# Performance work log

Measured on AMD Instinct MI355X. Metric: run time of the kernel, lower is better.

## Reference

```python
import jax, jax.numpy as jnp
import numpy as np

B, S = 2, 2048
HID, NH, NKV, HD = 4096, 32, 8, 128
THETA = 10000.0
WINDOW = 1024  # sliding window size


def setup_inputs() -> dict:
    key = jax.random.key(0)
    k1, k2, k3 = jax.random.split(key, 3)
    hidden_states = jax.random.normal(k1, (B, S, HID), jnp.float32)
    wqkv = jax.random.normal(k2, (HID, (NH + 2 * NKV) * HD), jnp.float32) * 0.02
    wo = jax.random.normal(k3, (NH * HD, HID), jnp.float32) * 0.02
    positions = jnp.arange(S, dtype=jnp.int32)
    return {"hidden_states": hidden_states, "wqkv": wqkv, "wo": wo, "positions": positions}


def _rope_neox(x, positions):
    # x: [B, S, h, HD]; GPT-NeoX style: rotate concatenated halves.
    half = HD // 2
    inv_freq = 1.0 / (THETA ** (jnp.arange(half, dtype=jnp.float32) / half))
    ang = positions.astype(jnp.float32)[:, None] * inv_freq  # [S, half]
    cos = jnp.cos(ang)[None, :, None, :]
    sin = jnp.sin(ang)[None, :, None, :]
    x1, x2 = jnp.split(x, 2, axis=-1)
    return jnp.concatenate([x1 * cos - x2 * sin, x2 * cos + x1 * sin], axis=-1)


def reference(hidden_states, wqkv, wo, positions):
    qkv = hidden_states @ wqkv  # [B, S, (NH+2*NKV)*HD]
    q, k, v = jnp.split(qkv, [NH * HD, NH * HD + NKV * HD], axis=-1)
    q = q.reshape(B, S, NH, HD)
    k = k.reshape(B, S, NKV, HD)
    v = v.reshape(B, S, NKV, HD)
    q = _rope_neox(q, positions)
    k = _rope_neox(k, positions)
    # GQA: each KV head serves NH // NKV query heads
    rep = NH // NKV
    k = jnp.repeat(k, rep, axis=2)  # [B, S, NH, HD]
    v = jnp.repeat(v, rep, axis=2)
    scale = HD ** -0.5
    scores = jnp.einsum('bqhd,bkhd->bhqk', q, k) * scale  # [B, NH, S, S]
    i = jnp.arange(S)[:, None]
    j = jnp.arange(S)[None, :]
    mask = (j <= i) & (i - j < WINDOW)  # causal + sliding window
    scores = jnp.where(mask[None, None], scores, jnp.float32(-1e30))
    probs = jax.nn.softmax(scores, axis=-1)
    attn = jnp.einsum('bhqk,bkhd->bqhd', probs, v).reshape(B, S, NH * HD)
    return attn @ wo  # [B, S, HID]
```

## Files before the change

kernel.cpp:

```cpp
#include <hip/hip_runtime.h>


typedef __attribute__((ext_vector_type(8))) short short8;
typedef __attribute__((ext_vector_type(4))) float f32x4;
typedef __attribute__((ext_vector_type(16))) float f32x16;
typedef __attribute__((ext_vector_type(4))) unsigned int u32x4;
typedef __attribute__((ext_vector_type(4))) unsigned short u16x4;

__device__ __forceinline__ unsigned short f2bf(float f) {
  unsigned int u = __builtin_bit_cast(unsigned int, f);
  u = u + 0x7fffu + ((u >> 16) & 1u);
  return (unsigned short)(u >> 16);
}
__device__ __forceinline__ float bf2f(unsigned short h) {
  unsigned int u = ((unsigned int)h) << 16;
  return __builtin_bit_cast(float, u);
}
__device__ __forceinline__ unsigned int cvtpk_bf16(float lo, float hi) {
  unsigned int r;
  asm("v_cvt_pk_bf16_f32 %0, %1, %2" : "=v"(r) : "v"(lo), "v"(hi));
  return r;
}

__device__ __forceinline__ void gload_lds16(const unsigned short* g, unsigned short* l) {
  __builtin_amdgcn_global_load_lds(
      (const __attribute__((address_space(1))) unsigned int*)g,
      (__attribute__((address_space(3))) unsigned int*)l, 16, 0, 0);
}

#define MFMA16(A, B, C) __builtin_amdgcn_mfma_f32_16x16x32_bf16((A), (B), (C), 0, 0, 0)
#define MFMA32(A, B, C) __builtin_amdgcn_mfma_f32_32x32x16_bf16((A), (B), (C), 0, 0, 0)
#define BC8(x) __builtin_bit_cast(short8, (x))

__global__ __launch_bounds__(256) void cvt_plain(const float* __restrict__ in,
                                                 unsigned short* __restrict__ out, int n) {
  const int i = (blockIdx.x * 256 + threadIdx.x) * 4;
  (void)n;
  f32x4 v = *(const f32x4*)(in + i);
  u16x4 o;
#pragma unroll
  for (int j = 0; j < 4; ++j) o[j] = f2bf(v[j]);
  *(u16x4*)(out + i) = o;
}

__global__ __launch_bounds__(256) void cvt_t(const float* __restrict__ in,
                                             unsigned short* __restrict__ out,
                                             int R, int C) {
  __shared__ float t[32][33];
  const int c0 = blockIdx.x * 32, r0 = blockIdx.y * 32;
  const int tx = threadIdx.x & 31, ty = threadIdx.x >> 5;
#pragma unroll
  for (int i = 0; i < 4; ++i)
    t[ty + i * 8][tx] = in[(size_t)(r0 + ty + i * 8) * C + c0 + tx];
  __syncthreads();
#pragma unroll
  for (int i = 0; i < 4; ++i)
    out[(size_t)(c0 + ty + i * 8) * R + r0 + tx] = f2bf(t[tx][ty + i * 8]);
}

template <int OUTF32>
__global__ __launch_bounds__(512, 2) void gemm256(const unsigned short* __restrict__ A,
                                                  const unsigned short* __restrict__ BT,
                                                  void* __restrict__ Cout,
                                                  int M, int N, int K) {
  __shared__ __align__(16) unsigned short lds[2][32768];
  const int tid = threadIdx.x;
  const int lane = tid & 63;
  const int w = tid >> 6;
  const int wr = w >> 2;
  const int wc = w & 3;
  const int g = lane >> 4;
  const int l15 = lane & 15;
  const int m0 = blockIdx.x * 256;
  const int n0 = blockIdx.y * 256;

  const int lrow = lane >> 3;
  const int lcol = ((lane & 7) ^ lrow) * 8;
  const unsigned short* Asrc = A + (size_t)(m0 + w * 8 + lrow) * K + lcol;
  const unsigned short* Bsrc = BT + (size_t)(n0 + w * 8 + lrow) * K + lcol;

  f32x4 acc[8][4] = {};

  auto stage = [&](int buf, int t, int r) {
    const int rb = (r < 4) ? (r * 64) : ((r & 1) * 128 + ((r >> 1) & 1) * 64);
    const unsigned short* src = ((r >= 4) ? Asrc : Bsrc) + (size_t)rb * K + t * 64;
    unsigned short* dst = &lds[buf][((r >= 4) ? 0 : 16384) + (rb + w * 8) * 64];
    gload_lds16(src, dst);
  };
  auto rdA = [&](int buf, int mi, int ks) {
    const int row = wr * 128 + mi * 16 + l15;
    const int cb = (ks * 64 + g * 16) ^ ((l15 & 7) << 4);
    return *(const u32x4*)((const char*)&lds[buf][0] + row * 128 + cb);
  };
  auto rdB = [&](int buf, int ni, int ks) {
    const int row = wc * 64 + ni * 16 + l15;
    const int cb = (ks * 64 + g * 16) ^ ((l15 & 7) << 4);
    return *(const u32x4*)((const char*)&lds[buf][16384] + row * 128 + cb);
  };

#pragma unroll
  for (int r = 0; r < 8; ++r) stage(0, 0, r);
  asm volatile("s_waitcnt vmcnt(2)" ::: "memory");
  __builtin_amdgcn_sched_barrier(0);
  __builtin_amdgcn_s_barrier();

  const int NT = K >> 6;
  for (int t = 0; t < NT; ++t) {
    const int cb_ = t & 1, nb_ = cb_ ^ 1;
    const bool pre = (t + 1 < NT);
    u32x4 bfr[4][2];

    {
#pragma unroll
      for (int ni = 0; ni < 4; ++ni) {
        bfr[ni][0] = rdB(cb_, ni, 0);
        bfr[ni][1] = rdB(cb_, ni, 1);
      }
      u32x4 a00 = rdA(cb_, 0, 0), a01 = rdA(cb_, 0, 1);
      u32x4 a10 = rdA(cb_, 1, 0), a11 = rdA(cb_, 1, 1);
      if (pre) { stage(nb_, t + 1, 0); stage(nb_, t + 1, 1); }
      __builtin_amdgcn_sched_barrier(0);
      __builtin_amdgcn_s_barrier();
      asm volatile("s_waitcnt lgkmcnt(0)" ::: "memory");
      __builtin_amdgcn_sched_barrier(0);
      __builtin_amdgcn_s_setprio(1);
#pragma unroll
      for (int ni = 0; ni < 4; ++ni) {
        acc[0][ni] = MFMA16(BC8(a00), BC8(bfr[ni][0]), acc[0][ni]);
        acc[0][ni] = MFMA16(BC8(a01), BC8(bfr[ni][1]), acc[0][ni]);
        acc[1][ni] = MFMA16(BC8(a10), BC8(bfr[ni][0]), acc[1][ni]);
        acc[1][ni] = MFMA16(BC8(a11), BC8(bfr[ni][1]), acc[1][ni]);
      }
      __builtin_amdgcn_s_setprio(0);
      __builtin_amdgcn_sched_barrier(0);
      __builtin_amdgcn_s_barrier();
    }
    {
      u32x4 a00 = rdA(cb_, 2, 0), a01 = rdA(cb_, 2, 1);
      u32x4 a10 = rdA(cb_, 3, 0), a11 = rdA(cb_, 3, 1);
      if (pre) {
        stage(nb_, t + 1, 2); stage(nb_, t + 1, 3);
        asm volatile("s_waitcnt vmcnt(4)" ::: "memory");
      } else {
        asm volatile("s_waitcnt vmcnt(0)" ::: "memory");
      }
      __builtin_amdgcn_sched_barrier(0);
      __builtin_amdgcn_s_barrier();
      asm volatile("s_waitcnt lgkmcnt(0)" ::: "memory");
      __builtin_amdgcn_sched_barrier(0);
      __builtin_amdgcn_s_setprio(1);
#pragma unroll
      for (int ni = 0; ni < 4; ++ni) {
        acc[2][ni] = MFMA16(BC8(a00), BC8(bfr[ni][0]), acc[2][ni]);
        acc[2][ni] = MFMA16(BC8(a01), BC8(bfr[ni][1]), acc[2][ni]);
        acc[3][ni] = MFMA16(BC8(a10), BC8(bfr[ni][0]), acc[3][ni]);
        acc[3][ni] = MFMA16(BC8(a11), BC8(bfr[ni][1]), acc[3][ni]);
      }
      __builtin_amdgcn_s_setprio(0);
      __builtin_amdgcn_sched_barrier(0);
      __builtin_amdgcn_s_barrier();
    }
    {
      u32x4 a00 = rdA(cb_, 4, 0), a01 = rdA(cb_, 4, 1);
      u32x4 a10 = rdA(cb_, 5, 0), a11 = rdA(cb_, 5, 1);
      if (pre) { stage(nb_, t + 1, 4); stage(nb_, t + 1, 5); }
      __builtin_amdgcn_sched_barrier(0);
      __builtin_amdgcn_s_barrier();
      asm volatile("s_waitcnt lgkmcnt(0)" ::: "memory");
      __builtin_amdgcn_sched_barrier(0);
      __builtin_amdgcn_s_setprio(1);
#pragma unroll
      for (int ni = 0; ni < 4; ++ni) {
        acc[4][ni] = MFMA16(BC8(a00), BC8(bfr[ni][0]), acc[4][ni]);
        acc[4][ni] = MFMA16(BC8(a01), BC8(bfr[ni][1]), acc[4][ni]);
        acc[5][ni] = MFMA16(BC8(a10), BC8(bfr[ni][0]), acc[5][ni]);
        acc[5][ni] = MFMA16(BC8(a11), BC8(bfr[ni][1]), acc[5][ni]);
      }
      __builtin_amdgcn_s_setprio(0);
      __builtin_amdgcn_sched_barrier(0);
      __builtin_amdgcn_s_barrier();
    }
    {
      u32x4 a00 = rdA(cb_, 6, 0), a01 = rdA(cb_, 6, 1);
      u32x4 a10 = rdA(cb_, 7, 0), a11 = rdA(cb_, 7, 1);
      if (pre) {
        stage(nb_, t + 1, 6); stage(nb_, t + 1, 7);
        asm volatile("s_waitcnt vmcnt(2)" ::: "memory");
      }
      __builtin_amdgcn_sched_barrier(0);
      __builtin_amdgcn_s_barrier();
      asm volatile("s_waitcnt lgkmcnt(0)" ::: "memory");
      __builtin_amdgcn_sched_barrier(0);
      __builtin_amdgcn_s_setprio(1);
#pragma unroll
      for (int ni = 0; ni < 4; ++ni) {
        acc[6][ni] = MFMA16(BC8(a00), BC8(bfr[ni][0]), acc[6][ni]);
        acc[6][ni] = MFMA16(BC8(a01), BC8(bfr[ni][1]), acc[6][ni]);
        acc[7][ni] = MFMA16(BC8(a10), BC8(bfr[ni][0]), acc[7][ni]);
        acc[7][ni] = MFMA16(BC8(a11), BC8(bfr[ni][1]), acc[7][ni]);
      }
      __builtin_amdgcn_s_setprio(0);
      __builtin_amdgcn_sched_barrier(0);
      __builtin_amdgcn_s_barrier();
    }
  }

  const int crow0 = m0 + wr * 128;
  const int ccol0 = n0 + wc * 64;
#pragma unroll
  for (int mi = 0; mi < 8; ++mi)
#pragma unroll
    for (int ni = 0; ni < 4; ++ni)
#pragma unroll
      for (int r = 0; r < 4; ++r) {
        const size_t idx =
            (size_t)(crow0 + mi * 16 + g * 4 + r) * N + (ccol0 + ni * 16 + l15);
        if constexpr (OUTF32) ((float*)Cout)[idx] = acc[mi][ni][r];
        else ((unsigned short*)Cout)[idx] = f2bf(acc[mi][ni][r]);
      }
}

__global__ __launch_bounds__(256) void rope_kernel(unsigned short* __restrict__ qkv,
                                                   const int* __restrict__ pos) {
  const int idx = blockIdx.x * 256 + threadIdx.x;
  const int d = idx & 63;
  const int hh = (idx >> 6) % 40;
  const int tok = idx / 2560;
  const int s = tok & 2047;
  const int off = (hh < 32) ? hh * 128 : 4096 + (hh - 32) * 128;
  unsigned short* p = qkv + (size_t)tok * 6144 + off + d;
  const float x1 = bf2f(p[0]);
  const float x2 = bf2f(p[64]);
  const float inv = exp2f(-(float)d * 0.2076205059304601f);
  const float ang = (float)pos[s] * inv;
  const float c = cosf(ang), sn = sinf(ang);
  p[0]  = f2bf(x1 * c - x2 * sn);
  p[64] = f2bf(x2 * c + x1 * sn);
}

__global__ __launch_bounds__(512, 2) void attn_kernel(const unsigned short* __restrict__ qkv,
                                                      unsigned short* __restrict__ aout) {
  __shared__ __align__(16) unsigned short smem[35840];

  const int tid = threadIdx.x;
  const int lane = tid & 63;
  const int w = tid >> 6;
  const int hi = lane >> 5;
  const int l31 = lane & 31;
  const int q0 = blockIdx.x * 256;
  const int h = blockIdx.y;
  const int b = blockIdx.z;
  const int kh = h >> 2;
  const size_t tokbase = (size_t)b * 2048;
  const int qw0 = q0 + w * 32;
  const int qg = qw0 + l31;

  short8 qf[8];
  {
    const unsigned short* qp = qkv + (tokbase + qg) * 6144 + h * 128;
#pragma unroll
    for (int ks8 = 0; ks8 < 8; ++ks8)
      qf[ks8] = BC8(*(const u32x4*)(qp + ks8 * 16 + hi * 8));
  }

  const int c0key = tid >> 4, c0col = tid & 15;
  const int c1key = (tid + 512) >> 4, c1col = tid & 15;

  u32x4 kreg[2], vreg[2];
  const unsigned short* kvK = qkv + tokbase * 6144 + 4096 + kh * 128;

  const int t0 = (q0 >= 1024 ? (q0 - 1023) >> 6 : 0);
  const int t1 = (q0 + 255) >> 6;

  {
    const unsigned short* kb = kvK + (size_t)(t0 * 64) * 6144;
    kreg[0] = *(const u32x4*)(kb + (size_t)c0key * 6144 + c0col * 8);
    kreg[1] = *(const u32x4*)(kb + (size_t)c1key * 6144 + c1col * 8);
    vreg[0] = *(const u32x4*)(kb + (size_t)c0key * 6144 + 1024 + c0col * 8);
    vreg[1] = *(const u32x4*)(kb + (size_t)c1key * 6144 + 1024 + c1col * 8);
  }

  float m_run = -1e30f, l_run = 0.0f;
  f32x16 o_acc[4] = {};

  for (int kt = t0; kt <= t1; ++kt) {
    const int cur = (kt - t0) & 1;
    unsigned short* kdst = &smem[(cur)*17920];
    unsigned short* vdst = kdst + 8704;

    if (kt == t0) {
      *(u32x4*)&kdst[c0key * 136 + c0col * 8] = kreg[0];
      *(u32x4*)&kdst[c1key * 136 + c1col * 8] = kreg[1];
#pragma unroll
      for (int e = 0; e < 8; ++e) {
        const int e0 = (e + c0col) & 7;
        const int e1 = (e + c1col) & 7;
        vdst[(c0col * 8 + e0) * 72 + c0key] =
            (unsigned short)(vreg[0][e0 >> 1] >> ((e0 & 1) * 16));
        vdst[(c1col * 8 + e1) * 72 + c1key] =
            (unsigned short)(vreg[1][e1 >> 1] >> ((e1 & 1) * 16));
      }
      if (kt < t1) {
        const unsigned short* kb = kvK + (size_t)((kt + 1) * 64) * 6144;
        kreg[0] = *(const u32x4*)(kb + (size_t)c0key * 6144 + c0col * 8);
        kreg[1] = *(const u32x4*)(kb + (size_t)c1key * 6144 + c1col * 8);
        vreg[0] = *(const u32x4*)(kb + (size_t)c0key * 6144 + 1024 + c0col * 8);
        vreg[1] = *(const u32x4*)(kb + (size_t)c1key * 6144 + 1024 + c1col * 8);
      }
      __syncthreads();
    }

    if (kt < t1) {
      unsigned short* kdn = &smem[(cur ^ 1) * 17920];
      unsigned short* vdn = kdn + 8704;
      *(u32x4*)&kdn[c0key * 136 + c0col * 8] = kreg[0];
      *(u32x4*)&kdn[c1key * 136 + c1col * 8] = kreg[1];
#pragma unroll
      for (int e = 0; e < 8; ++e) {
        const int e0 = (e + c0col) & 7;
        const int e1 = (e + c1col) & 7;
        vdn[(c0col * 8 + e0) * 72 + c0key] =
            (unsigned short)(vreg[0][e0 >> 1] >> ((e0 & 1) * 16));
        vdn[(c1col * 8 + e1) * 72 + c1key] =
            (unsigned short)(vreg[1][e1 >> 1] >> ((e1 & 1) * 16));
      }
      if (kt + 2 <= t1) {
        const unsigned short* kb = kvK + (size_t)((kt + 2) * 64) * 6144;
        kreg[0] = *(const u32x4*)(kb + (size_t)c0key * 6144 + c0col * 8);
        kreg[1] = *(const u32x4*)(kb + (size_t)c1key * 6144 + c1col * 8);
        vreg[0] = *(const u32x4*)(kb + (size_t)c0key * 6144 + 1024 + c0col * 8);
        vreg[1] = *(const u32x4*)(kb + (size_t)c1key * 6144 + 1024 + c1col * 8);
      }
    }

    const int ktb = kt * 64;
    if (ktb <= qw0 + 31 && ktb + 63 >= qw0 - 1023) {
      const unsigned short* kb = &smem[cur * 17920];
      const unsigned short* vb = kb + 8704;

      f32x16 s0 = {}, s1 = {};
      const int arow = l31 * 136 + hi * 8;
#pragma unroll
      for (int ks8 = 0; ks8 < 8; ++ks8) {
        u32x4 a0 = *(const u32x4*)&kb[arow + ks8 * 16];
        u32x4 a1 = *(const u32x4*)&kb[arow + 32 * 136 + ks8 * 16];
        s0 = MFMA32(BC8(a0), qf[ks8], s0);
        s1 = MFMA32(BC8(a1), qf[ks8], s1);
      }

      const float scale = 0.08838834764831845f;
      float pv[32];
      const bool need_mask = !(ktb + 63 <= qw0 && ktb >= qw0 - 992);
      if (need_mask) {
#pragma unroll
        for (int r = 0; r < 16; ++r) {
          const int key0 = ktb + ((r & 3) + 8 * (r >> 2) + 4 * hi);
          const int key1 = key0 + 32;
          pv[r]      = (key0 <= qg && qg - key0 < 1024) ? s0[r] * scale : -1e30f;
          pv[16 + r] = (key1 <= qg && qg - key1 < 1024) ? s1[r] * scale : -1e30f;
        }
      } else {
#pragma unroll
        for (int r = 0; r < 16; ++r) {
          pv[r] = s0[r] * scale;
          pv[16 + r] = s1[r] * scale;
        }
      }

      float tm = -1e30f;
#pragma unroll
      for (int i = 0; i < 32; ++i) tm = fmaxf(tm, pv[i]);
      tm = fmaxf(tm, __shfl_xor(tm, 32, 64));
      if (__any(tm > m_run + 8.0f)) {
        const float mn = fmaxf(fmaxf(m_run, tm), -1e20f);
        const float scl = __expf(m_run - mn);
#pragma unroll
        for (int d = 0; d < 4; ++d) o_acc[d] *= scl;
        l_run *= scl;
        m_run = mn;
      }
      float lsum = 0.0f;
#pragma unroll
      for (int i = 0; i < 32; ++i) {
        pv[i] = __expf(pv[i] - m_run);
        lsum += pv[i];
      }
      l_run += lsum + __shfl_xor(lsum, 32, 64);

      u32x4 paf[4];
#pragma unroll
      for (int ks = 0; ks < 4; ++ks) {
        const int base = (ks >> 1) * 16 + (ks & 1) * 8;
        auto rA = __builtin_amdgcn_permlane32_swap(
            (int)cvtpk_bf16(pv[base + 0], pv[base + 1]),
            (int)cvtpk_bf16(pv[base + 4], pv[base + 5]), false, false);
        auto rB = __builtin_amdgcn_permlane32_swap(
            (int)cvtpk_bf16(pv[base + 2], pv[base + 3]),
            (int)cvtpk_bf16(pv[base + 6], pv[base + 7]), false, false);
        paf[ks][0] = (unsigned int)rA[0];
        paf[ks][1] = (unsigned int)rB[0];
        paf[ks][2] = (unsigned int)rA[1];
        paf[ks][3] = (unsigned int)rB[1];
      }

#pragma unroll
      for (int dblk = 0; dblk < 4; ++dblk) {
        const int vrow = (dblk * 32 + l31) * 72 + hi * 8;
#pragma unroll
        for (int ks = 0; ks < 4; ++ks) {
          u32x4 vf = *(const u32x4*)&vb[vrow + ks * 16];
          o_acc[dblk] = MFMA32(BC8(vf), BC8(paf[ks]), o_acc[dblk]);
        }
      }
    }

    __syncthreads();
  }

  const float rl = 1.0f / l_run;
  unsigned short* ob = &smem[w * 4352];
#pragma unroll
  for (int dblk = 0; dblk < 4; ++dblk)
#pragma unroll
    for (int rq = 0; rq < 4; ++rq) {
      u16x4 pk;
#pragma unroll
      for (int i = 0; i < 4; ++i) pk[i] = f2bf(o_acc[dblk][rq * 4 + i] * rl);
      *(u16x4*)&ob[l31 * 136 + dblk * 32 + rq * 8 + hi * 4] = pk;
    }
  __syncthreads();

  unsigned short* gout = aout + (tokbase + q0 + w * 32) * 4096 + h * 128;
#pragma unroll
  for (int r4 = 0; r4 < 8; ++r4) {
    const int row = r4 * 4 + (lane >> 4);
    u32x4 val = *(const u32x4*)&ob[row * 136 + (lane & 15) * 8];
    *(u32x4*)(gout + (size_t)row * 4096 + (lane & 15) * 8) = val;
  }
}

extern "C" void kernel_launch(void* const* d_in, const int* in_sizes, int n_in,
                              void* d_out, int out_size, void* d_ws, size_t ws_size,
                              hipStream_t stream) {
  (void)in_sizes; (void)n_in; (void)out_size; (void)ws_size;
  const float* hs   = (const float*)d_in[0];
  const float* wqkv = (const float*)d_in[1];
  const float* wo   = (const float*)d_in[2];
  const int*   pos  = (const int*)d_in[3];
  float* out = (float*)d_out;

  char* ws = (char*)d_ws;
  unsigned short* qkvb = (unsigned short*)ws;
  unsigned short* wT   = (unsigned short*)(ws + 50331648);
  unsigned short* hsb  = (unsigned short*)(ws + 100663296);

  cvt_t<<<dim3(6144 / 32, 4096 / 32), 256, 0, stream>>>(wqkv, wT, 4096, 6144);
  cvt_plain<<<16384, 256, 0, stream>>>(hs, hsb, 16777216);
  gemm256<0><<<dim3(16, 24), 512, 0, stream>>>(hsb, wT, qkvb, 4096, 6144, 4096);
  rope_kernel<<<40960, 256, 0, stream>>>(qkvb, pos);
  cvt_t<<<dim3(4096 / 32, 4096 / 32), 256, 0, stream>>>(wo, wT, 4096, 4096);
  attn_kernel<<<dim3(8, 32, 2), 512, 0, stream>>>(qkvb, hsb);
  gemm256<1><<<dim3(16, 16), 512, 0, stream>>>(hsb, wT, out, 4096, 4096, 4096);
}
```

Measured before the change: 536.0 us.

## Swizzle GEMM tiles across XCDs and XOR-swizzle attention K/V LDS layout

The GEMM kernels switch to a 1D grid whose block index is remapped so that consecutive tiles land on the same XCD (bid&7 groups), aiming for better L2 reuse of A/B panels. The attention kernel replaces its padded K/V shared-memory layout (row strides 136/72) with dense rows addressed through an XOR swizzle, reducing bank conflicts on the MFMA operand reads and transposed V writes. LDS use in attention grows slightly to 72KB, which still allows two 512-thread blocks per CU, and the stage-index expression is rewritten in an equivalent form.

```diff
diff --git a/kernel.cpp b/kernel.cpp
--- a/kernel.cpp
+++ b/kernel.cpp
@@ -71,8 +71,14 @@
   const int wc = w & 3;
   const int g = lane >> 4;
   const int l15 = lane & 15;
-  const int m0 = blockIdx.x * 256;
-  const int n0 = blockIdx.y * 256;
+
+  const int nwg = gridDim.x;
+  const int cpx = nwg >> 3;
+  const int bid = blockIdx.x;
+  const int swz = (bid & 7) * cpx + (bid >> 3);
+  const int MT = M >> 8;
+  const int m0 = (swz % MT) * 256;
+  const int n0 = (swz / MT) * 256;
 
   const int lrow = lane >> 3;
   const int lcol = ((lane & 7) ^ lrow) * 8;
@@ -82,7 +88,7 @@
   f32x4 acc[8][4] = {};
 
   auto stage = [&](int buf, int t, int r) {
-    const int rb = (r < 4) ? (r * 64) : ((r & 1) * 128 + ((r >> 1) & 1) * 64);
+    const int rb = (r < 4) ? (r * 64) : (((r - 4) & 1) * 128 + (((r - 4) >> 1) & 1) * 64);
     const unsigned short* src = ((r >= 4) ? Asrc : Bsrc) + (size_t)rb * K + t * 64;
     unsigned short* dst = &lds[buf][((r >= 4) ? 0 : 16384) + (rb + w * 8) * 64];
     gload_lds16(src, dst);
@@ -95,7 +101,7 @@
   auto rdB = [&](int buf, int ni, int ks) {
     const int row = wc * 64 + ni * 16 + l15;
     const int cb = (ks * 64 + g * 16) ^ ((l15 & 7) << 4);
-    return *(const u32x4*)((const char*)&lds[buf][16384] + row * 128 + cb);
+    return *(const u32x4*)((const char*)&lds[buf][0] + 32768 + row * 128 + cb);
   };
 
 #pragma unroll
@@ -240,7 +246,7 @@
 
 __global__ __launch_bounds__(512, 2) void attn_kernel(const unsigned short* __restrict__ qkv,
                                                       unsigned short* __restrict__ aout) {
-  __shared__ __align__(16) unsigned short smem[35840];
+  __shared__ __align__(16) unsigned char smem[73728];
 
   const int tid = threadIdx.x;
   const int lane = tid & 63;
@@ -254,6 +260,7 @@
   const size_t tokbase = (size_t)b * 2048;
   const int qw0 = q0 + w * 32;
   const int qg = qw0 + l31;
+  const int sw = (l31 & 7) << 4;
 
   short8 qf[8];
   {
@@ -264,7 +271,7 @@
   }
 
   const int c0key = tid >> 4, c0col = tid & 15;
-  const int c1key = (tid + 512) >> 4, c1col = tid & 15;
+  const int c1key = c0key + 32;
 
   u32x4 kreg[2], vreg[2];
   const unsigned short* kvK = qkv + tokbase * 6144 + 4096 + kh * 128;
@@ -275,75 +282,60 @@
   {
     const unsigned short* kb = kvK + (size_t)(t0 * 64) * 6144;
     kreg[0] = *(const u32x4*)(kb + (size_t)c0key * 6144 + c0col * 8);
-    kreg[1] = *(const u32x4*)(kb + (size_t)c1key * 6144 + c1col * 8);
+    kreg[1] = *(const u32x4*)(kb + (size_t)c1key * 6144 + c0col * 8);
     vreg[0] = *(const u32x4*)(kb + (size_t)c0key * 6144 + 1024 + c0col * 8);
-    vreg[1] = *(const u32x4*)(kb + (size_t)c1key * 6144 + 1024 + c1col * 8);
+    vreg[1] = *(const u32x4*)(kb + (size_t)c1key * 6144 + 1024 + c0col * 8);
   }
+
+  auto write_kv = [&](unsigned char* base) {
+    *(u32x4*)(base + ((c0key * 256 + c0col * 16) ^ ((c0key & 7) << 4))) = kreg[0];
+    *(u32x4*)(base + ((c1key * 256 + c0col * 16) ^ ((c1key & 7) << 4))) = kreg[1];
+    unsigned char* vd = base + 16384;
+#pragma unroll
+    for (int e = 0; e < 8; ++e) {
+      const int e0 = (e + c0col) & 7;
+      const int d = c0col * 8 + e0;
+      *(unsigned short*)(vd + (((d * 128) + c0key * 2) ^ (e0 << 4))) =
+          (unsigned short)(vreg[0][e0 >> 1] >> ((e0 & 1) * 16));
+      *(unsigned short*)(vd + (((d * 128) + c1key * 2) ^ (e0 << 4))) =
+          (unsigned short)(vreg[1][e0 >> 1] >> ((e0 & 1) * 16));
+    }
+  };
+  auto load_kv = [&](int kt) {
+    const unsigned short* kb = kvK + (size_t)(kt * 64) * 6144;
+    kreg[0] = *(const u32x4*)(kb + (size_t)c0key * 6144 + c0col * 8);
+    kreg[1] = *(const u32x4*)(kb + (size_t)c1key * 6144 + c0col * 8);
+    vreg[0] = *(const u32x4*)(kb + (size_t)c0key * 6144 + 1024 + c0col * 8);
+    vreg[1] = *(const u32x4*)(kb + (size_t)c1key * 6144 + 1024 + c0col * 8);
+  };
 
   float m_run = -1e30f, l_run = 0.0f;
   f32x16 o_acc[4] = {};
 
   for (int kt = t0; kt <= t1; ++kt) {
     const int cur = (kt - t0) & 1;
-    unsigned short* kdst = &smem[(cur)*17920];
-    unsigned short* vdst = kdst + 8704;
 
     if (kt == t0) {
-      *(u32x4*)&kdst[c0key * 136 + c0col * 8] = kreg[0];
-      *(u32x4*)&kdst[c1key * 136 + c1col * 8] = kreg[1];
-#pragma unroll
-      for (int e = 0; e < 8; ++e) {
-        const int e0 = (e + c0col) & 7;
-        const int e1 = (e + c1col) & 7;
-        vdst[(c0col * 8 + e0) * 72 + c0key] =
-            (unsigned short)(vreg[0][e0 >> 1] >> ((e0 & 1) * 16));
-        vdst[(c1col * 8 + e1) * 72 + c1key] =
-            (unsigned short)(vreg[1][e1 >> 1] >> ((e1 & 1) * 16));
-      }
-      if (kt < t1) {
-        const unsigned short* kb = kvK + (size_t)((kt + 1) * 64) * 6144;
-        kreg[0] = *(const u32x4*)(kb + (size_t)c0key * 6144 + c0col * 8);
-        kreg[1] = *(const u32x4*)(kb + (size_t)c1key * 6144 + c1col * 8);
-        vreg[0] = *(const u32x4*)(kb + (size_t)c0key * 6144 + 1024 + c0col * 8);
-        vreg[1] = *(const u32x4*)(kb + (size_t)c1key * 6144 + 1024 + c1col * 8);
-      }
+      write_kv(smem + cur * 32768);
+      if (kt < t1) load_kv(kt + 1);
       __syncthreads();
     }
 
     if (kt < t1) {
-      unsigned short* kdn = &smem[(cur ^ 1) * 17920];
-      unsigned short* vdn = kdn + 8704;
-      *(u32x4*)&kdn[c0key * 136 + c0col * 8] = kreg[0];
-      *(u32x4*)&kdn[c1key * 136 + c1col * 8] = kreg[1];
-#pragma unroll
-      for (int e = 0; e < 8; ++e) {
-        const int e0 = (e + c0col) & 7;
-        const int e1 = (e + c1col) & 7;
-        vdn[(c0col * 8 + e0) * 72 + c0key] =
-            (unsigned short)(vreg[0][e0 >> 1] >> ((e0 & 1) * 16));
-        vdn[(c1col * 8 + e1) * 72 + c1key] =
-            (unsigned short)(vreg[1][e1 >> 1] >> ((e1 & 1) * 16));
-      }
-      if (kt + 2 <= t1) {
-        const unsigned short* kb = kvK + (size_t)((kt + 2) * 64) * 6144;
-        kreg[0] = *(const u32x4*)(kb + (size_t)c0key * 6144 + c0col * 8);
-        kreg[1] = *(const u32x4*)(kb + (size_t)c1key * 6144 + c1col * 8);
-        vreg[0] = *(const u32x4*)(kb + (size_t)c0key * 6144 + 1024 + c0col * 8);
-        vreg[1] = *(const u32x4*)(kb + (size_t)c1key * 6144 + 1024 + c1col * 8);
-      }
+      write_kv(smem + (cur ^ 1) * 32768);
+      if (kt + 2 <= t1) load_kv(kt + 2);
     }
 
     const int ktb = kt * 64;
     if (ktb <= qw0 + 31 && ktb + 63 >= qw0 - 1023) {
-      const unsigned short* kb = &smem[cur * 17920];
-      const unsigned short* vb = kb + 8704;
+      const unsigned char* kb = smem + cur * 32768;
+      const unsigned char* vb = kb + 16384;
 
       f32x16 s0 = {}, s1 = {};
-      const int arow = l31 * 136 + hi * 8;
 #pragma unroll
       for (int ks8 = 0; ks8 < 8; ++ks8) {
-        u32x4 a0 = *(const u32x4*)&kb[arow + ks8 * 16];
-        u32x4 a1 = *(const u32x4*)&kb[arow + 32 * 136 + ks8 * 16];
+        u32x4 a0 = *(const u32x4*)(kb + ((l31 * 256 + ks8 * 32 + hi * 16) ^ sw));
+        u32x4 a1 = *(const u32x4*)(kb + (((32 + l31) * 256 + ks8 * 32 + hi * 16) ^ sw));
         s0 = MFMA32(BC8(a0), qf[ks8], s0);
         s1 = MFMA32(BC8(a1), qf[ks8], s1);
       }
@@ -405,10 +397,10 @@
 
 #pragma unroll
       for (int dblk = 0; dblk < 4; ++dblk) {
-        const int vrow = (dblk * 32 + l31) * 72 + hi * 8;
 #pragma unroll
         for (int ks = 0; ks < 4; ++ks) {
-          u32x4 vf = *(const u32x4*)&vb[vrow + ks * 16];
+          u32x4 vf = *(const u32x4*)(vb +
+              (((dblk * 32 + l31) * 128 + ks * 32 + hi * 16) ^ sw));
           o_acc[dblk] = MFMA32(BC8(vf), BC8(paf[ks]), o_acc[dblk]);
         }
       }
@@ -418,7 +410,7 @@
   }
 
   const float rl = 1.0f / l_run;
-  unsigned short* ob = &smem[w * 4352];
+  unsigned char* ob = smem + w * 8704;
 #pragma unroll
   for (int dblk = 0; dblk < 4; ++dblk)
 #pragma unroll
@@ -426,7 +418,7 @@
       u16x4 pk;
 #pragma unroll
       for (int i = 0; i < 4; ++i) pk[i] = f2bf(o_acc[dblk][rq * 4 + i] * rl);
-      *(u16x4*)&ob[l31 * 136 + dblk * 32 + rq * 8 + hi * 4] = pk;
+      *(u16x4*)(ob + l31 * 272 + (dblk * 32 + rq * 8 + hi * 4) * 2) = pk;
     }
   __syncthreads();
 
@@ -434,7 +426,7 @@
 #pragma unroll
   for (int r4 = 0; r4 < 8; ++r4) {
     const int row = r4 * 4 + (lane >> 4);
-    u32x4 val = *(const u32x4*)&ob[row * 136 + (lane & 15) * 8];
+    u32x4 val = *(const u32x4*)(ob + row * 272 + (lane & 15) * 16);
     *(u32x4*)(gout + (size_t)row * 4096 + (lane & 15) * 8) = val;
   }
 }
@@ -456,9 +448,9 @@
 
   cvt_t<<<dim3(6144 / 32, 4096 / 32), 256, 0, stream>>>(wqkv, wT, 4096, 6144);
   cvt_plain<<<16384, 256, 0, stream>>>(hs, hsb, 16777216);
-  gemm256<0><<<dim3(16, 24), 512, 0, stream>>>(hsb, wT, qkvb, 4096, 6144, 4096);
+  gemm256<0><<<384, 512, 0, stream>>>(hsb, wT, qkvb, 4096, 6144, 4096);
   rope_kernel<<<40960, 256, 0, stream>>>(qkvb, pos);
   cvt_t<<<dim3(4096 / 32, 4096 / 32), 256, 0, stream>>>(wo, wT, 4096, 4096);
   attn_kernel<<<dim3(8, 32, 2), 512, 0, stream>>>(qkvb, hsb);
-  gemm256<1><<<dim3(16, 16), 512, 0, stream>>>(hsb, wT, out, 4096, 4096, 4096);
-}
+  gemm256<1><<<256, 512, 0, stream>>>(hsb, wT, out, 4096, 4096, 4096);
+}
```

Result: slower. 546.8 us (+2.0%).
